# Kernel tuning notes

Hardware: AMD Instinct MI355X
Metric: run time of the kernel (lower is better)

The kernel has to match this reference:

```python
import jax, jax.numpy as jnp
import numpy as np

TOP_K = 2
LB_WEIGHT = 0.01
Z_WEIGHT = 0.001


def setup_inputs() -> dict:
    key = jax.random.key(0)
    ks = jax.random.split(key, 5)
    B, S, D, F, E = 4, 2048, 1024, 2048, 8
    x = jax.random.normal(ks[0], (B, S, D), dtype=jnp.float32)
    Wr = jax.random.normal(ks[1], (D, E), dtype=jnp.float32) / np.sqrt(D).astype(np.float32)
    Wg = jax.random.normal(ks[2], (E, D, F), dtype=jnp.float32) / np.sqrt(D).astype(np.float32)
    Wu = jax.random.normal(ks[3], (E, D, F), dtype=jnp.float32) / np.sqrt(D).astype(np.float32)
    Wd = jax.random.normal(ks[4], (E, F, D), dtype=jnp.float32) / np.sqrt(F).astype(np.float32)
    return {"x": x, "Wr": Wr, "Wg": Wg, "Wu": Wu, "Wd": Wd}


def reference(x, Wr, Wg, Wu, Wd):
    B, S, D = x.shape
    E = Wr.shape[1]
    xf = x.reshape(-1, D)                       # [T, D]
    T = xf.shape[0]

    logits = xf @ Wr                            # [T, E]
    probs = jax.nn.softmax(logits, axis=-1)
    topv, topi = jax.lax.top_k(probs, TOP_K)    # [T, K]
    topv = topv / jnp.sum(topv, axis=-1, keepdims=True)

    # combine[t, e] = renormalized top-k prob if expert e selected for token t, else 0
    onehot = jax.nn.one_hot(topi, E, dtype=x.dtype)          # [T, K, E]
    combine = jnp.sum(onehot * topv[..., None], axis=1)      # [T, E]

    out = jnp.zeros_like(xf)
    for e in range(E):  # fixed small expert count; dense compute masked by combine weights
        h = jax.nn.silu(xf @ Wg[e]) * (xf @ Wu[e])           # [T, F] SwiGLU
        out = out + combine[:, e:e + 1] * (h @ Wd[e])

    # auxiliary losses
    counts = jnp.sum(onehot, axis=(0, 1))                    # [E] tokens routed per expert
    f_i = counts / (T * TOP_K)
    P_i = jnp.mean(probs, axis=0)
    load_balance = E * jnp.sum(f_i * P_i)
    z_loss = jnp.mean(jax.nn.logsumexp(logits, axis=-1) ** 2)
    aux_loss = LB_WEIGHT * load_balance + Z_WEIGHT * z_loss

    return out.reshape(B, S, D), aux_loss
```

## Files before the change

### kernel.cpp

```cpp
#include <hip/hip_runtime.h>
#include <cstdint>

#define T_TOK 8192
#define Dm 1024
#define Fm 2048
#define Em 8

typedef unsigned short u16;
typedef __attribute__((ext_vector_type(8))) short short8;
typedef __attribute__((ext_vector_type(4))) float floatx4;

__device__ __forceinline__ u16 f2bf(float f) {
  union { float f; unsigned u; } v; v.f = f;
  unsigned r = v.u + 0x7fffu + ((v.u >> 16) & 1u);
  return (u16)(r >> 16);
}

__device__ __forceinline__ void gld_lds16(const void* g, void* l) {
  __builtin_amdgcn_global_load_lds(
      (const __attribute__((address_space(1))) void*)g,
      (__attribute__((address_space(3))) void*)l, 16, 0, 0);
}

__global__ void zero_meta(int* counts, int* offc, float* psum, float* zsum) {
  int t = threadIdx.x;
  if (t < 8) { counts[t] = 0; offc[t] = 0; psum[t] = 0.f; }
  if (t == 8) zsum[0] = 0.f;
}

__global__ __launch_bounds__(256) void prep_kernel(
    const float* __restrict__ Wg, const float* __restrict__ Wu, const float* __restrict__ Wd,
    u16* __restrict__ WgT, u16* __restrict__ WuT, u16* __restrict__ WdT,
    const float* __restrict__ x, const float* __restrict__ Wr, u16* __restrict__ xb,
    int* __restrict__ topi, float* __restrict__ topw,
    int* __restrict__ counts, float* __restrict__ psum, float* __restrict__ zsum) {
  __shared__ __align__(16) char smem[33056];
  int tid = threadIdx.x;
  if (blockIdx.x < 24 * 512) {
    u16* tile = (u16*)smem;
    int bid = blockIdx.x;
    int m = bid >> 9, t = bid & 511;
    int type = m >> 3, e = m & 7;
    const float* src; u16* dst; int R, C, csh;
    if (type == 0)      { src = Wg; dst = WgT; R = Dm; C = Fm; csh = 5; }
    else if (type == 1) { src = Wu; dst = WuT; R = Dm; C = Fm; csh = 5; }
    else                { src = Wd; dst = WdT; R = Fm; C = Dm; csh = 4; }
    int ty = t >> csh, tx = t & ((1 << csh) - 1);
    int r0 = ty * 64, c0 = tx * 64;
    const float* s = src + (size_t)e * R * C;
    u16* d = dst + (size_t)e * C * R;
#pragma unroll
    for (int p = 0; p < 16; ++p) {
      int idx = p * 256 + tid;
      int i = idx >> 6, j = idx & 63;
      tile[i * 66 + j] = f2bf(s[(size_t)(r0 + i) * C + (c0 + j)]);
    }
    __syncthreads();
#pragma unroll
    for (int p = 0; p < 16; ++p) {
      int idx = p * 256 + tid;
      int i = idx >> 6, j = idx & 63;
      d[(size_t)(c0 + i) * R + (r0 + j)] = tile[j * 66 + i];
    }
    return;
  }
  int rb = blockIdx.x - 24 * 512;
  float* wr_s = (float*)smem;
  float (*redf)[9] = (float(*)[9])(smem + 32768);
  int (*redi)[8] = (int(*)[8])(smem + 32768 + 144);
  for (int i = tid; i < Dm * Em; i += 256) wr_s[i] = Wr[i];
  __syncthreads();
  int wv = tid >> 6, lane = tid & 63;
  float pl[8] = {0, 0, 0, 0, 0, 0, 0, 0};
  float zl = 0.f;
  int cl[8] = {0, 0, 0, 0, 0, 0, 0, 0};
  for (int it = 0; it < 8; ++it) {
    int t = (rb * 4 + wv) * 8 + it;
    const float* xt = x + (size_t)t * Dm;
    u16* xbt = xb + (size_t)t * Dm;
    float acc[8] = {0, 0, 0, 0, 0, 0, 0, 0};
#pragma unroll
    for (int i = 0; i < 16; ++i) {
      int dd = i * 64 + lane;
      float xv = xt[dd];
      xbt[dd] = f2bf(xv);
#pragma unroll
      for (int e2 = 0; e2 < 8; ++e2) acc[e2] += xv * wr_s[dd * 8 + e2];
    }
#pragma unroll
    for (int e2 = 0; e2 < 8; ++e2) {
      float v = acc[e2];
      for (int o = 32; o > 0; o >>= 1) v += __shfl_down(v, o);
      acc[e2] = v;
    }
    if (lane == 0) {
      float m = acc[0];
#pragma unroll
      for (int e2 = 1; e2 < 8; ++e2) m = fmaxf(m, acc[e2]);
      float p[8]; float s = 0.f;
#pragma unroll
      for (int e2 = 0; e2 < 8; ++e2) { p[e2] = expf(acc[e2] - m); s += p[e2]; }
      float inv = 1.f / s;
#pragma unroll
      for (int e2 = 0; e2 < 8; ++e2) { p[e2] *= inv; pl[e2] += p[e2]; }
      float lse = m + logf(s);
      zl += lse * lse;
      int i1 = 0;
#pragma unroll
      for (int e2 = 1; e2 < 8; ++e2) if (p[e2] > p[i1]) i1 = e2;
      int i2 = -1; float b2 = -1e30f;
#pragma unroll
      for (int e2 = 0; e2 < 8; ++e2)
        if (e2 != i1 && p[e2] > b2) { b2 = p[e2]; i2 = e2; }
      float ssum = p[i1] + p[i2];
      topi[2 * t] = i1; topi[2 * t + 1] = i2;
      topw[2 * t] = p[i1] / ssum; topw[2 * t + 1] = p[i2] / ssum;
      cl[i1]++; cl[i2]++;
    }
  }
  if (lane == 0) {
#pragma unroll
    for (int e2 = 0; e2 < 8; ++e2) { redf[wv][e2] = pl[e2]; redi[wv][e2] = cl[e2]; }
    redf[wv][8] = zl;
  }
  __syncthreads();
  if (tid < 8) {
    atomicAdd(&psum[tid], redf[0][tid] + redf[1][tid] + redf[2][tid] + redf[3][tid]);
    atomicAdd(&counts[tid], redi[0][tid] + redi[1][tid] + redi[2][tid] + redi[3][tid]);
  } else if (tid == 8) {
    atomicAdd(zsum, redf[0][8] + redf[1][8] + redf[2][8] + redf[3][8]);
  }
}

__global__ __launch_bounds__(256) void scatter_kernel(
    const int* __restrict__ topi, const float* __restrict__ topw,
    const int* __restrict__ counts, const float* __restrict__ psum, const float* __restrict__ zsum,
    int* __restrict__ offc, int* __restrict__ etok, float* __restrict__ ew,
    int* __restrict__ slots, float* __restrict__ out_aux) {
  __shared__ int lcnt[8];
  __shared__ int lbase[8];
  __shared__ int basesS[8];
  int tid = threadIdx.x;
  if (blockIdx.x == 0 && tid == 0) {
    float lb = 0.f;
    for (int e = 0; e < 8; ++e)
      lb += ((float)counts[e] / (2.f * T_TOK)) * (psum[e] / (float)T_TOK);
    lb *= 8.f;
    float z = zsum[0] / (float)T_TOK;
    *out_aux = 0.01f * lb + 0.001f * z;
  }
  if (tid < 8) {
    lcnt[tid] = 0;
    int b = 0;
    for (int e = 0; e < tid; ++e) b += counts[e];
    basesS[tid] = b;
  }
  __syncthreads();
  int t = blockIdx.x * 256 + tid;
  int e0 = topi[2 * t], e1 = topi[2 * t + 1];
  int lp0 = atomicAdd(&lcnt[e0], 1);
  int lp1 = atomicAdd(&lcnt[e1], 1);
  __syncthreads();
  if (tid < 8) lbase[tid] = atomicAdd(&offc[tid], lcnt[tid]);
  __syncthreads();
  int p0 = basesS[e0] + lbase[e0] + lp0;
  etok[p0] = t; ew[p0] = topw[2 * t]; slots[2 * t] = p0;
  int p1 = basesS[e1] + lbase[e1] + lp1;
  etok[p1] = t; ew[p1] = topw[2 * t + 1]; slots[2 * t + 1] = p1;
}

__global__ void bases_kernel(const int* counts, int* bases) {
  if (threadIdx.x == 0) {
    int b = 0;
    for (int e = 0; e < 8; ++e) { bases[e] = b; b += counts[e]; }
  }
}

__global__ __launch_bounds__(256, 2) void gemm1_kernel(
    const u16* __restrict__ xb, const u16* __restrict__ WgT, const u16* __restrict__ WuT,
    u16* __restrict__ h, const int* __restrict__ etok,
    const int* __restrict__ counts, const int* __restrict__ bases) {
  const int e = blockIdx.z;
  const int Ne = counts[e];
  const int m0 = blockIdx.y * 128;
  if (m0 >= Ne) return;
  const int n0 = blockIdx.x * 128;
  const int be = bases[e];

  __shared__ __align__(16) u16 As[128 * 64];
  __shared__ __align__(16) u16 Bgs[128 * 64];
  __shared__ __align__(16) u16 Bus[128 * 64];

  const int tid = threadIdx.x;
  const int wv = tid >> 6, lane = tid & 63;
  const int wr = wv >> 1, wc = wv & 1;
  const int srow = tid >> 3;
  const int cg = (tid & 7) ^ (srow & 7);
  const u16* wg_e = WgT + (size_t)e * Fm * Dm;
  const u16* wu_e = WuT + (size_t)e * Fm * Dm;

  const u16* ag[4]; const u16* bgp[4]; const u16* bup[4];
#pragma unroll
  for (int j = 0; j < 4; ++j) {
    int row = 32 * j + srow;
    int rr = m0 + row; rr = rr < Ne ? rr : Ne - 1;
    int tok = etok[be + rr];
    ag[j] = xb + (size_t)tok * Dm + cg * 8;
    bgp[j] = wg_e + (size_t)(n0 + row) * Dm + cg * 8;
    bup[j] = wu_e + (size_t)(n0 + row) * Dm + cg * 8;
  }
  const int lbase = 8 * wv * 64 + lane * 8;

  floatx4 accg[4][4], accu[4][4];
#pragma unroll
  for (int mi = 0; mi < 4; ++mi)
#pragma unroll
    for (int ni = 0; ni < 4; ++ni) { accg[mi][ni] = (floatx4)0.f; accu[mi][ni] = (floatx4)0.f; }

  for (int k0 = 0; k0 < Dm; k0 += 64) {
    __syncthreads();
#pragma unroll
    for (int j = 0; j < 4; ++j) {
      int lo = lbase + 32 * j * 64;
      gld_lds16(ag[j] + k0, &As[lo]);
      gld_lds16(bgp[j] + k0, &Bgs[lo]);
      gld_lds16(bup[j] + k0, &Bus[lo]);
    }
    __syncthreads();
#pragma unroll
    for (int ks = 0; ks < 2; ++ks) {
      short8 af[4], bgf[4], buf_[4];
      const int col = lane & 15, quad = lane >> 4;
      const int c = ks * 4 + quad;
#pragma unroll
      for (int mi = 0; mi < 4; ++mi) {
        int row = wr * 64 + mi * 16 + col;
        af[mi] = *(const short8*)&As[row * 64 + ((c ^ (row & 7)) << 3)];
      }
#pragma unroll
      for (int ni = 0; ni < 4; ++ni) {
        int row = wc * 64 + ni * 16 + col;
        int o = row * 64 + ((c ^ (row & 7)) << 3);
        bgf[ni] = *(const short8*)&Bgs[o];
        buf_[ni] = *(const short8*)&Bus[o];
      }
#pragma unroll
      for (int mi = 0; mi < 4; ++mi)
#pragma unroll
        for (int ni = 0; ni < 4; ++ni) {
          accg[mi][ni] = __builtin_amdgcn_mfma_f32_16x16x32_bf16(af[mi], bgf[ni], accg[mi][ni], 0, 0, 0);
          accu[mi][ni] = __builtin_amdgcn_mfma_f32_16x16x32_bf16(af[mi], buf_[ni], accu[mi][ni], 0, 0, 0);
        }
    }
  }
  const int col = lane & 15, quad = lane >> 4;
#pragma unroll
  for (int mi = 0; mi < 4; ++mi)
#pragma unroll
    for (int ni = 0; ni < 4; ++ni) {
      int f = n0 + wc * 64 + ni * 16 + col;
#pragma unroll
      for (int r = 0; r < 4; ++r) {
        int lrow = wr * 64 + mi * 16 + quad * 4 + r;
        if (m0 + lrow < Ne) {
          float gv = accg[mi][ni][r];
          float hv = (gv / (1.f + expf(-gv))) * accu[mi][ni][r];
          h[(size_t)(be + m0 + lrow) * Fm + f] = f2bf(hv);
        }
      }
    }
}

__global__ __launch_bounds__(256, 2) void gemm2_kernel(
    const u16* __restrict__ h, const u16* __restrict__ WdT, float* __restrict__ h2,
    const float* __restrict__ ew,
    const int* __restrict__ counts, const int* __restrict__ bases) {
  const int e = blockIdx.z;
  const int Ne = counts[e];
  const int m0 = blockIdx.y * 128;
  if (m0 >= Ne) return;
  const int n0 = blockIdx.x * 128;
  const int be = bases[e];

  __shared__ __align__(16) u16 As[128 * 64];
  __shared__ __align__(16) u16 Bs[128 * 64];
  __shared__ float wS[128];

  const int tid = threadIdx.x;
  if (tid < 128) {
    int rr = m0 + tid; rr = rr < Ne ? rr : Ne - 1;
    wS[tid] = ew[be + rr];
  }
  const int wv = tid >> 6, lane = tid & 63;
  const int wr = wv >> 1, wc = wv & 1;
  const int srow = tid >> 3;
  const int cg = (tid & 7) ^ (srow & 7);
  const u16* wd_e = WdT + (size_t)e * Dm * Fm;

  const u16* ap[4]; const u16* bp[4];
#pragma unroll
  for (int j = 0; j < 4; ++j) {
    int row = 32 * j + srow;
    int rr = m0 + row; rr = rr < Ne ? rr : Ne - 1;
    ap[j] = h + (size_t)(be + rr) * Fm + cg * 8;
    bp[j] = wd_e + (size_t)(n0 + row) * Fm + cg * 8;
  }
  const int lbase = 8 * wv * 64 + lane * 8;

  floatx4 acc[4][4];
#pragma unroll
  for (int mi = 0; mi < 4; ++mi)
#pragma unroll
    for (int ni = 0; ni < 4; ++ni) acc[mi][ni] = (floatx4)0.f;

  for (int k0 = 0; k0 < Fm; k0 += 64) {
    __syncthreads();
#pragma unroll
    for (int j = 0; j < 4; ++j) {
      int lo = lbase + 32 * j * 64;
      gld_lds16(ap[j] + k0, &As[lo]);
      gld_lds16(bp[j] + k0, &Bs[lo]);
    }
    __syncthreads();
#pragma unroll
    for (int ks = 0; ks < 2; ++ks) {
      short8 af[4], bf[4];
      const int col = lane & 15, quad = lane >> 4;
      const int c = ks * 4 + quad;
#pragma unroll
      for (int mi = 0; mi < 4; ++mi) {
        int row = wr * 64 + mi * 16 + col;
        af[mi] = *(const short8*)&As[row * 64 + ((c ^ (row & 7)) << 3)];
      }
#pragma unroll
      for (int ni = 0; ni < 4; ++ni) {
        int row = wc * 64 + ni * 16 + col;
        bf[ni] = *(const short8*)&Bs[row * 64 + ((c ^ (row & 7)) << 3)];
      }
#pragma unroll
      for (int mi = 0; mi < 4; ++mi)
#pragma unroll
        for (int ni = 0; ni < 4; ++ni)
          acc[mi][ni] = __builtin_amdgcn_mfma_f32_16x16x32_bf16(af[mi], bf[ni], acc[mi][ni], 0, 0, 0);
    }
  }
  const int col = lane & 15, quad = lane >> 4;
#pragma unroll
  for (int mi = 0; mi < 4; ++mi)
#pragma unroll
    for (int ni = 0; ni < 4; ++ni) {
      int oc = n0 + wc * 64 + ni * 16 + col;
#pragma unroll
      for (int r = 0; r < 4; ++r) {
        int lrow = wr * 64 + mi * 16 + quad * 4 + r;
        if (m0 + lrow < Ne)
          h2[(size_t)(be + m0 + lrow) * Dm + oc] = acc[mi][ni][r] * wS[lrow];
      }
    }
}

__global__ __launch_bounds__(256) void combine_kernel(
    const float* __restrict__ h2, const int* __restrict__ slots, float* __restrict__ out) {
  int t = blockIdx.x;
  int d4 = threadIdx.x;
  int s0 = slots[2 * t], s1 = slots[2 * t + 1];
  const float4* r0 = (const float4*)(h2 + (size_t)s0 * Dm);
  const float4* r1 = (const float4*)(h2 + (size_t)s1 * Dm);
  float4 a = r0[d4], b = r1[d4];
  float4 o = make_float4(a.x + b.x, a.y + b.y, a.z + b.z, a.w + b.w);
  ((float4*)(out + (size_t)t * Dm))[d4] = o;
}

extern "C" void kernel_launch(void* const* d_in, const int* in_sizes, int n_in,
                              void* d_out, int out_size, void* d_ws, size_t ws_size,
                              hipStream_t stream) {
  const float* x = (const float*)d_in[0];
  const float* Wr = (const float*)d_in[1];
  const float* Wg = (const float*)d_in[2];
  const float* Wu = (const float*)d_in[3];
  const float* Wd = (const float*)d_in[4];
  float* out = (float*)d_out;

  char* p = (char*)d_ws;
  auto take = [&](size_t bytes) { char* r = p; p += (bytes + 255) & ~(size_t)255; return r; };
  u16* WgT = (u16*)take((size_t)Em * Fm * Dm * 2);
  u16* WuT = (u16*)take((size_t)Em * Fm * Dm * 2);
  u16* WdT = (u16*)take((size_t)Em * Dm * Fm * 2);
  u16* xb = (u16*)take((size_t)T_TOK * Dm * 2);
  u16* gh = (u16*)take((size_t)2 * T_TOK * Fm * 2);
  int* topi = (int*)take((size_t)T_TOK * 2 * 4);
  float* topw = (float*)take((size_t)T_TOK * 2 * 4);
  int* etok = (int*)take((size_t)2 * T_TOK * 4);
  float* ew = (float*)take((size_t)2 * T_TOK * 4);
  int* slots = (int*)take((size_t)2 * T_TOK * 4);
  int* counts = (int*)take(64);
  int* bases = (int*)take(64);
  int* offc = (int*)take(64);
  float* psum = (float*)take(64);
  float* zsum = (float*)take(64);
  float* h2 = (float*)WgT;

  zero_meta<<<1, 64, 0, stream>>>(counts, offc, psum, zsum);
  prep_kernel<<<dim3(24 * 512 + 256), 256, 0, stream>>>(
      Wg, Wu, Wd, WgT, WuT, WdT, x, Wr, xb, topi, topw, counts, psum, zsum);
  scatter_kernel<<<dim3(T_TOK / 256), 256, 0, stream>>>(
      topi, topw, counts, psum, zsum, offc, etok, ew, slots, out + (size_t)T_TOK * Dm);
  bases_kernel<<<1, 64, 0, stream>>>(counts, bases);
  gemm1_kernel<<<dim3(Fm / 128, 64, Em), 256, 0, stream>>>(xb, WgT, WuT, gh, etok, counts, bases);
  gemm2_kernel<<<dim3(Dm / 128, 64, Em), 256, 0, stream>>>(gh, WdT, h2, ew, counts, bases);
  combine_kernel<<<dim3(T_TOK), 256, 0, stream>>>(h2, slots, out);
}
```

Measured before the change: 561.4 us.

## Halve GEMM N-tile to 64, raise occupancy, fold bases into scatter, reorder prep blocks

Both expert GEMMs drop from 128x128 to 128x64 output tiles, with smaller B staging buffers and fewer accumulators, and launch bounds move from 2 to 3 blocks per SM. This doubles the grid and raises occupancy, aimed at filling the CUs better when per-expert token counts are uneven. The cost is less reuse of the A tile and more redundant loads of gathered tokens. The separate bases kernel is removed, with scatter block 0 writing the bases instead, and prep now runs the routing blocks first so they are scheduled ahead of the weight-transpose blocks.

```diff
diff --git a/kernel.cpp b/kernel.cpp
--- a/kernel.cpp
+++ b/kernel.cpp
@@ -36,9 +36,9 @@
     int* __restrict__ counts, float* __restrict__ psum, float* __restrict__ zsum) {
   __shared__ __align__(16) char smem[33056];
   int tid = threadIdx.x;
-  if (blockIdx.x < 24 * 512) {
+  if (blockIdx.x >= 256) {
     u16* tile = (u16*)smem;
-    int bid = blockIdx.x;
+    int bid = blockIdx.x - 256;
     int m = bid >> 9, t = bid & 511;
     int type = m >> 3, e = m & 7;
     const float* src; u16* dst; int R, C, csh;
@@ -64,7 +64,7 @@
     }
     return;
   }
-  int rb = blockIdx.x - 24 * 512;
+  int rb = blockIdx.x;
   float* wr_s = (float*)smem;
   float (*redf)[9] = (float(*)[9])(smem + 32768);
   int (*redi)[8] = (int(*)[8])(smem + 32768 + 144);
@@ -136,7 +136,7 @@
     const int* __restrict__ topi, const float* __restrict__ topw,
     const int* __restrict__ counts, const float* __restrict__ psum, const float* __restrict__ zsum,
     int* __restrict__ offc, int* __restrict__ etok, float* __restrict__ ew,
-    int* __restrict__ slots, float* __restrict__ out_aux) {
+    int* __restrict__ slots, int* __restrict__ bases, float* __restrict__ out_aux) {
   __shared__ int lcnt[8];
   __shared__ int lbase[8];
   __shared__ int basesS[8];
@@ -154,6 +154,7 @@
     int b = 0;
     for (int e = 0; e < tid; ++e) b += counts[e];
     basesS[tid] = b;
+    if (blockIdx.x == 0) bases[tid] = b;
   }
   __syncthreads();
   int t = blockIdx.x * 256 + tid;
@@ -169,14 +170,7 @@
   etok[p1] = t; ew[p1] = topw[2 * t + 1]; slots[2 * t + 1] = p1;
 }
 
-__global__ void bases_kernel(const int* counts, int* bases) {
-  if (threadIdx.x == 0) {
-    int b = 0;
-    for (int e = 0; e < 8; ++e) { bases[e] = b; b += counts[e]; }
-  }
-}
-
-__global__ __launch_bounds__(256, 2) void gemm1_kernel(
+__global__ __launch_bounds__(256, 3) void gemm1_kernel(
     const u16* __restrict__ xb, const u16* __restrict__ WgT, const u16* __restrict__ WuT,
     u16* __restrict__ h, const int* __restrict__ etok,
     const int* __restrict__ counts, const int* __restrict__ bases) {
@@ -184,12 +178,12 @@
   const int Ne = counts[e];
   const int m0 = blockIdx.y * 128;
   if (m0 >= Ne) return;
-  const int n0 = blockIdx.x * 128;
+  const int n0 = blockIdx.x * 64;
   const int be = bases[e];
 
   __shared__ __align__(16) u16 As[128 * 64];
-  __shared__ __align__(16) u16 Bgs[128 * 64];
-  __shared__ __align__(16) u16 Bus[128 * 64];
+  __shared__ __align__(16) u16 Bgs[64 * 64];
+  __shared__ __align__(16) u16 Bus[64 * 64];
 
   const int tid = threadIdx.x;
   const int wv = tid >> 6, lane = tid & 63;
@@ -199,37 +193,42 @@
   const u16* wg_e = WgT + (size_t)e * Fm * Dm;
   const u16* wu_e = WuT + (size_t)e * Fm * Dm;
 
-  const u16* ag[4]; const u16* bgp[4]; const u16* bup[4];
+  const u16* ag[4]; const u16* bgp[2]; const u16* bup[2];
 #pragma unroll
   for (int j = 0; j < 4; ++j) {
     int row = 32 * j + srow;
     int rr = m0 + row; rr = rr < Ne ? rr : Ne - 1;
     int tok = etok[be + rr];
     ag[j] = xb + (size_t)tok * Dm + cg * 8;
+  }
+#pragma unroll
+  for (int j = 0; j < 2; ++j) {
+    int row = 32 * j + srow;
     bgp[j] = wg_e + (size_t)(n0 + row) * Dm + cg * 8;
     bup[j] = wu_e + (size_t)(n0 + row) * Dm + cg * 8;
   }
   const int lbase = 8 * wv * 64 + lane * 8;
 
-  floatx4 accg[4][4], accu[4][4];
+  floatx4 accg[4][2], accu[4][2];
 #pragma unroll
   for (int mi = 0; mi < 4; ++mi)
 #pragma unroll
-    for (int ni = 0; ni < 4; ++ni) { accg[mi][ni] = (floatx4)0.f; accu[mi][ni] = (floatx4)0.f; }
+    for (int ni = 0; ni < 2; ++ni) { accg[mi][ni] = (floatx4)0.f; accu[mi][ni] = (floatx4)0.f; }
 
   for (int k0 = 0; k0 < Dm; k0 += 64) {
     __syncthreads();
 #pragma unroll
-    for (int j = 0; j < 4; ++j) {
+    for (int j = 0; j < 4; ++j) gld_lds16(ag[j] + k0, &As[lbase + 32 * j * 64]);
+#pragma unroll
+    for (int j = 0; j < 2; ++j) {
       int lo = lbase + 32 * j * 64;
-      gld_lds16(ag[j] + k0, &As[lo]);
       gld_lds16(bgp[j] + k0, &Bgs[lo]);
       gld_lds16(bup[j] + k0, &Bus[lo]);
     }
     __syncthreads();
 #pragma unroll
     for (int ks = 0; ks < 2; ++ks) {
-      short8 af[4], bgf[4], buf_[4];
+      short8 af[4], bgf[2], buf_[2];
       const int col = lane & 15, quad = lane >> 4;
       const int c = ks * 4 + quad;
 #pragma unroll
@@ -238,8 +237,8 @@
         af[mi] = *(const short8*)&As[row * 64 + ((c ^ (row & 7)) << 3)];
       }
 #pragma unroll
-      for (int ni = 0; ni < 4; ++ni) {
-        int row = wc * 64 + ni * 16 + col;
+      for (int ni = 0; ni < 2; ++ni) {
+        int row = wc * 32 + ni * 16 + col;
         int o = row * 64 + ((c ^ (row & 7)) << 3);
         bgf[ni] = *(const short8*)&Bgs[o];
         buf_[ni] = *(const short8*)&Bus[o];
@@ -247,7 +246,7 @@
 #pragma unroll
       for (int mi = 0; mi < 4; ++mi)
 #pragma unroll
-        for (int ni = 0; ni < 4; ++ni) {
+        for (int ni = 0; ni < 2; ++ni) {
           accg[mi][ni] = __builtin_amdgcn_mfma_f32_16x16x32_bf16(af[mi], bgf[ni], accg[mi][ni], 0, 0, 0);
           accu[mi][ni] = __builtin_amdgcn_mfma_f32_16x16x32_bf16(af[mi], buf_[ni], accu[mi][ni], 0, 0, 0);
         }
@@ -257,8 +256,8 @@
 #pragma unroll
   for (int mi = 0; mi < 4; ++mi)
 #pragma unroll
-    for (int ni = 0; ni < 4; ++ni) {
-      int f = n0 + wc * 64 + ni * 16 + col;
+    for (int ni = 0; ni < 2; ++ni) {
+      int f = n0 + wc * 32 + ni * 16 + col;
 #pragma unroll
       for (int r = 0; r < 4; ++r) {
         int lrow = wr * 64 + mi * 16 + quad * 4 + r;
@@ -271,7 +270,7 @@
     }
 }
 
-__global__ __launch_bounds__(256, 2) void gemm2_kernel(
+__global__ __launch_bounds__(256, 3) void gemm2_kernel(
     const u16* __restrict__ h, const u16* __restrict__ WdT, float* __restrict__ h2,
     const float* __restrict__ ew,
     const int* __restrict__ counts, const int* __restrict__ bases) {
@@ -279,11 +278,11 @@
   const int Ne = counts[e];
   const int m0 = blockIdx.y * 128;
   if (m0 >= Ne) return;
-  const int n0 = blockIdx.x * 128;
+  const int n0 = blockIdx.x * 64;
   const int be = bases[e];
 
   __shared__ __align__(16) u16 As[128 * 64];
-  __shared__ __align__(16) u16 Bs[128 * 64];
+  __shared__ __align__(16) u16 Bs[64 * 64];
   __shared__ float wS[128];
 
   const int tid = threadIdx.x;
@@ -297,34 +296,36 @@
   const int cg = (tid & 7) ^ (srow & 7);
   const u16* wd_e = WdT + (size_t)e * Dm * Fm;
 
-  const u16* ap[4]; const u16* bp[4];
+  const u16* ap[4]; const u16* bp[2];
 #pragma unroll
   for (int j = 0; j < 4; ++j) {
     int row = 32 * j + srow;
     int rr = m0 + row; rr = rr < Ne ? rr : Ne - 1;
     ap[j] = h + (size_t)(be + rr) * Fm + cg * 8;
+  }
+#pragma unroll
+  for (int j = 0; j < 2; ++j) {
+    int row = 32 * j + srow;
     bp[j] = wd_e + (size_t)(n0 + row) * Fm + cg * 8;
   }
   const int lbase = 8 * wv * 64 + lane * 8;
 
-  floatx4 acc[4][4];
+  floatx4 acc[4][2];
 #pragma unroll
   for (int mi = 0; mi < 4; ++mi)
 #pragma unroll
-    for (int ni = 0; ni < 4; ++ni) acc[mi][ni] = (floatx4)0.f;
+    for (int ni = 0; ni < 2; ++ni) acc[mi][ni] = (floatx4)0.f;
 
   for (int k0 = 0; k0 < Fm; k0 += 64) {
     __syncthreads();
 #pragma unroll
-    for (int j = 0; j < 4; ++j) {
-      int lo = lbase + 32 * j * 64;
-      gld_lds16(ap[j] + k0, &As[lo]);
-      gld_lds16(bp[j] + k0, &Bs[lo]);
-    }
+    for (int j = 0; j < 4; ++j) gld_lds16(ap[j] + k0, &As[lbase + 32 * j * 64]);
+#pragma unroll
+    for (int j = 0; j < 2; ++j) gld_lds16(bp[j] + k0, &Bs[lbase + 32 * j * 64]);
     __syncthreads();
 #pragma unroll
     for (int ks = 0; ks < 2; ++ks) {
-      short8 af[4], bf[4];
+      short8 af[4], bf[2];
       const int col = lane & 15, quad = lane >> 4;
       const int c = ks * 4 + quad;
 #pragma unroll
@@ -333,14 +334,14 @@
         af[mi] = *(const short8*)&As[row * 64 + ((c ^ (row & 7)) << 3)];
       }
 #pragma unroll
-      for (int ni = 0; ni < 4; ++ni) {
-        int row = wc * 64 + ni * 16 + col;
+      for (int ni = 0; ni < 2; ++ni) {
+        int row = wc * 32 + ni * 16 + col;
         bf[ni] = *(const short8*)&Bs[row * 64 + ((c ^ (row & 7)) << 3)];
       }
 #pragma unroll
       for (int mi = 0; mi < 4; ++mi)
 #pragma unroll
-        for (int ni = 0; ni < 4; ++ni)
+        for (int ni = 0; ni < 2; ++ni)
           acc[mi][ni] = __builtin_amdgcn_mfma_f32_16x16x32_bf16(af[mi], bf[ni], acc[mi][ni], 0, 0, 0);
     }
   }
@@ -348,8 +349,8 @@
 #pragma unroll
   for (int mi = 0; mi < 4; ++mi)
 #pragma unroll
-    for (int ni = 0; ni < 4; ++ni) {
-      int oc = n0 + wc * 64 + ni * 16 + col;
+    for (int ni = 0; ni < 2; ++ni) {
+      int oc = n0 + wc * 32 + ni * 16 + col;
 #pragma unroll
       for (int r = 0; r < 4; ++r) {
         int lrow = wr * 64 + mi * 16 + quad * 4 + r;
@@ -404,9 +405,8 @@
   prep_kernel<<<dim3(24 * 512 + 256), 256, 0, stream>>>(
       Wg, Wu, Wd, WgT, WuT, WdT, x, Wr, xb, topi, topw, counts, psum, zsum);
   scatter_kernel<<<dim3(T_TOK / 256), 256, 0, stream>>>(
-      topi, topw, counts, psum, zsum, offc, etok, ew, slots, out + (size_t)T_TOK * Dm);
-  bases_kernel<<<1, 64, 0, stream>>>(counts, bases);
-  gemm1_kernel<<<dim3(Fm / 128, 64, Em), 256, 0, stream>>>(xb, WgT, WuT, gh, etok, counts, bases);
-  gemm2_kernel<<<dim3(Dm / 128, 64, Em), 256, 0, stream>>>(gh, WdT, h2, ew, counts, bases);
+      topi, topw, counts, psum, zsum, offc, etok, ew, slots, bases, out + (size_t)T_TOK * Dm);
+  gemm1_kernel<<<dim3(Fm / 64, 64, Em), 256, 0, stream>>>(xb, WgT, WuT, gh, etok, counts, bases);
+  gemm2_kernel<<<dim3(Dm / 64, 64, Em), 256, 0, stream>>>(gh, WdT, h2, ew, counts, bases);
   combine_kernel<<<dim3(T_TOK), 256, 0, stream>>>(h2, slots, out);
 }
```

New measurement: 522.4 us. 7.0% less time.
